# Kernel tuning notes

Hardware: AMD Instinct MI355X
Metric: run time of the kernel (lower is better)

The kernel has to match this reference:

```python
import jax, jax.numpy as jnp
import numpy as np

PERTURBATION_SCALE = 0.01

def setup_inputs() -> dict:
    key = jax.random.key(0)
    k1, k2, k3 = jax.random.split(key, 3)
    theta = jax.random.normal(k1, (256, 512), dtype=jnp.float32)
    basis_eval = jax.random.normal(k2, (100000, 512), dtype=jnp.float32)
    noise = jax.random.normal(k3, (256, 512), dtype=jnp.float32)
    return {"theta": theta, "basis_eval": basis_eval, "noise": noise}

def reference(theta, basis_eval, noise):
    # phi: [N, K] functional evaluations
    phi_raw = basis_eval @ theta.T
    phi_perturbed = basis_eval @ (theta + noise * PERTURBATION_SCALE).T
    # sign-crossings between consecutive evaluation points: [N-1, K]
    crossings = (phi_raw[:-1] * phi_raw[1:] < 0).astype(theta.dtype)
    crossings_p = (phi_perturbed[:-1] * phi_perturbed[1:] < 0).astype(theta.dtype)
    persistence = crossings * crossings_p  # [N-1, K]
    # fused pairwise shared-persistence: Gram matrix [K, K]
    gram = persistence.T @ persistence
    K = theta.shape[0]
    iu, ju = jnp.triu_indices(K, k=1)  # row-major i<j == itertools.combinations order
    return gram[iu, ju]  # [K*(K-1)/2]
```

## Files before the change

kernel.cpp:

```cpp
#include <hip/hip_runtime.h>
#include <hip/hip_bf16.h>
#include <stdint.h>

#define N_PTS   100000
#define D       512
#define KDIM    256
#define NB1     99999
#define NWORDS  1564
#define NW      1563
#define GRIDX   3128
#define CHUNK   391

typedef float  f32x4  __attribute__((ext_vector_type(4)));
typedef __bf16 bf16x8 __attribute__((ext_vector_type(8)));

__global__ void build_w(const float* __restrict__ theta,
                        const float* __restrict__ noise,
                        __bf16* __restrict__ W) {
    int idx = blockIdx.x * 256 + threadIdx.x;
    int j = idx >> 9;
    int d = idx & 511;
    float v;
    if (j < KDIM) v = theta[j * D + d];
    else          v = theta[(j - KDIM) * D + d] + 0.01f * noise[(j - KDIM) * D + d];
    W[idx] = (__bf16)v;
}

__global__ void __launch_bounds__(256)
gemm_signs(const float* __restrict__ basis,
           const __bf16* __restrict__ W,
           uint64_t* __restrict__ sbits) {
    __shared__ char smem[17024];
    __bf16* As = (__bf16*)smem;
    __bf16* Bs = (__bf16*)(smem + 8192);

    const int tid  = threadIdx.x;
    const int lane = tid & 63;
    const int wave = tid >> 6;
    const int wrow = wave >> 1;
    const int wcol = wave & 1;

    const int phys = blockIdx.x;
    const int lid  = (phys & 7) * CHUNK + (phys >> 3);
    const int bn   = lid & 3;
    const int bm   = lid >> 2;

    const int srow  = tid >> 1;
    const int shalf = tid & 1;
    int agrow = bm * 128 + srow;
    if (agrow > N_PTS - 1) agrow = N_PTS - 1;
    const float*  aptr = basis + (size_t)agrow * D + shalf * 16;
    const __bf16* bptr = W + (size_t)(bn * 128 + srow) * D + shalf * 16;

    f32x4 acc[4][4] = {};
    float4 ra[2][4];
    uint4  rb[2][2];

    {
        const float4* ap = (const float4*)aptr;
        ra[0][0] = ap[0]; ra[0][1] = ap[1]; ra[0][2] = ap[2]; ra[0][3] = ap[3];
        const uint4* bp = (const uint4*)bptr;
        rb[0][0] = bp[0]; rb[0][1] = bp[1];
    }

    const int lane16 = lane & 15;
    const int lgrp   = lane >> 4;
    const int aoff   = (wrow * 64 + lane16) * 32 + lgrp * 8;
    const int boff   = (wcol * 64 + lane16) * 32 + lgrp * 8;

    #pragma unroll
    for (int kt = 0; kt < 16; ++kt) {
        const int cur = kt & 1, nxt = cur ^ 1;

        if (kt < 15) {
            const float4* ap = (const float4*)(aptr + (size_t)(kt + 1) * 32);
            ra[nxt][0] = ap[0]; ra[nxt][1] = ap[1]; ra[nxt][2] = ap[2]; ra[nxt][3] = ap[3];
            const uint4* bp = (const uint4*)(bptr + (size_t)(kt + 1) * 32);
            rb[nxt][0] = bp[0]; rb[nxt][1] = bp[1];
        }

        __bf16 abuf[16];
        #pragma unroll
        for (int v = 0; v < 4; ++v) {
            abuf[v * 4 + 0] = (__bf16)ra[cur][v].x;
            abuf[v * 4 + 1] = (__bf16)ra[cur][v].y;
            abuf[v * 4 + 2] = (__bf16)ra[cur][v].z;
            abuf[v * 4 + 3] = (__bf16)ra[cur][v].w;
        }

        __builtin_amdgcn_s_barrier();
        {
            bf16x8* adst = (bf16x8*)&As[srow * 32 + shalf * 16];
            adst[0] = *(bf16x8*)&abuf[0];
            adst[1] = *(bf16x8*)&abuf[8];
            uint4* bdst = (uint4*)&Bs[srow * 32 + shalf * 16];
            bdst[0] = rb[cur][0];
            bdst[1] = rb[cur][1];
        }
        asm volatile("s_waitcnt lgkmcnt(0)" ::: "memory");
        __builtin_amdgcn_s_barrier();
        __builtin_amdgcn_sched_barrier(0);

        bf16x8 af[4], bfm[4];
        #pragma unroll
        for (int m = 0; m < 4; ++m) af[m]  = *(bf16x8*)&As[aoff + m * 512];
        #pragma unroll
        for (int n = 0; n < 4; ++n) bfm[n] = *(bf16x8*)&Bs[boff + n * 512];

        #pragma unroll
        for (int m = 0; m < 4; ++m)
            #pragma unroll
            for (int n = 0; n < 4; ++n)
                acc[m][n] = __builtin_amdgcn_mfma_f32_16x16x32_bf16(af[m], bfm[n], acc[m][n], 0, 0, 0);
    }

    __builtin_amdgcn_s_barrier();
    unsigned char* sb = (unsigned char*)smem;

    #pragma unroll
    for (int m = 0; m < 4; ++m) {
        #pragma unroll
        for (int n = 0; n < 4; ++n) {
            const int cl  = wcol * 64 + n * 16 + lane16;
            const int rw  = wrow * 64 + m * 16 + lgrp * 4;
            uint32_t pk = 0;
            #pragma unroll
            for (int r = 0; r < 4; ++r)
                pk |= (acc[m][n][r] < 0.0f ? 1u : 0u) << (8 * r);
            *(uint32_t*)&sb[cl * 132 + rw] = pk;
        }
    }
    asm volatile("s_waitcnt lgkmcnt(0)" ::: "memory");
    __builtin_amdgcn_s_barrier();

    {
        const int col  = tid >> 1;
        const int half = tid & 1;
        const unsigned char* src = &sb[col * 132 + half * 64];
        uint64_t wbits = 0;
        #pragma unroll
        for (int k = 0; k < 16; ++k) {
            uint32_t q  = *(const uint32_t*)&src[4 * k];
            uint32_t p4 = ((q & 0x01010101u) * 0x10204080u) >> 28;
            wbits |= (uint64_t)p4 << (4 * k);
        }
        sbits[(size_t)(bm * 2 + half) * 512 + bn * 128 + col] = wbits;
    }
}

__global__ void crossing_masks(const uint64_t* __restrict__ sbits,
                               uint64_t* __restrict__ maskT) {
    const int w = blockIdx.x;
    const int j = threadIdx.x;
    uint64_t s0r = sbits[(size_t)w * 512 + j];
    uint64_t s0p = sbits[(size_t)w * 512 + 256 + j];
    uint64_t s1r = sbits[(size_t)(w + 1) * 512 + j];
    uint64_t s1p = sbits[(size_t)(w + 1) * 512 + 256 + j];
    uint64_t cr = s0r ^ ((s0r >> 1) | (s1r << 63));
    uint64_t cp = s0p ^ ((s0p >> 1) | (s1p << 63));
    uint64_t m = cr & cp;
    if (w == NW - 1) m &= 0x7FFFFFFFull;
    maskT[(size_t)w * 256 + j] = m;
}

__global__ void zero_out(float* __restrict__ out) {
    int i = blockIdx.x * 256 + threadIdx.x;
    if (i < 32640) out[i] = 0.0f;
}

__global__ void pair_popcount(const uint64_t* __restrict__ maskT,
                              float* __restrict__ out) {
    const int i = blockIdx.x;
    const int c = blockIdx.y;
    const int j = threadIdx.x;
    if (j <= i) return;
    int w0 = c * 391;
    int w1 = w0 + 391; if (w1 > NW) w1 = NW;
    uint32_t sum = 0;
    #pragma unroll 4
    for (int w = w0; w < w1; ++w) {
        uint64_t mi = maskT[(size_t)w * 256 + i];
        uint64_t mj = maskT[(size_t)w * 256 + j];
        sum += (uint32_t)__popcll(mi & mj);
    }
    const size_t idx = (size_t)i * (2 * KDIM - i - 1) / 2 + (size_t)(j - i - 1);
    atomicAdd(&out[idx], (float)sum);
}

extern "C" void kernel_launch(void* const* d_in, const int* in_sizes, int n_in,
                              void* d_out, int out_size, void* d_ws, size_t ws_size,
                              hipStream_t stream) {
    const float* theta = (const float*)d_in[0];
    const float* basis = (const float*)d_in[1];
    const float* noise = (const float*)d_in[2];
    float* out = (float*)d_out;

    char* ws = (char*)d_ws;
    __bf16*   W     = (__bf16*)ws;
    uint64_t* sbits = (uint64_t*)(ws + 524288);
    uint64_t* maskT = (uint64_t*)(ws + 524288 + (size_t)NWORDS * 512 * 8);

    hipLaunchKernelGGL(build_w,        dim3(1024),    dim3(256), 0, stream, theta, noise, W);
    hipLaunchKernelGGL(gemm_signs,     dim3(GRIDX),   dim3(256), 0, stream, basis, W, sbits);
    hipLaunchKernelGGL(crossing_masks, dim3(NW),      dim3(256), 0, stream, sbits, maskT);
    hipLaunchKernelGGL(zero_out,       dim3(128),     dim3(256), 0, stream, out);
    hipLaunchKernelGGL(pair_popcount,  dim3(KDIM, 4), dim3(256), 0, stream, maskT, out);
}
```

Baseline: 143.2 us.

## Load GEMM fragments directly from global memory into registers, bypassing LDS staging

```diff
diff --git a/kernel.cpp b/kernel.cpp
--- a/kernel.cpp
+++ b/kernel.cpp
@@ -5,7 +5,6 @@
 #define N_PTS   100000
 #define D       512
 #define KDIM    256
-#define NB1     99999
 #define NWORDS  1564
 #define NW      1563
 #define GRIDX   3128
@@ -26,13 +25,11 @@
     W[idx] = (__bf16)v;
 }
 
-__global__ void __launch_bounds__(256)
+__global__ void __launch_bounds__(256, 2)
 gemm_signs(const float* __restrict__ basis,
            const __bf16* __restrict__ W,
            uint64_t* __restrict__ sbits) {
-    __shared__ char smem[17024];
-    __bf16* As = (__bf16*)smem;
-    __bf16* Bs = (__bf16*)(smem + 8192);
+    __shared__ unsigned char sb[128 * 132];
 
     const int tid  = threadIdx.x;
     const int lane = tid & 63;
@@ -45,67 +42,64 @@
     const int bn   = lid & 3;
     const int bm   = lid >> 2;
 
-    const int srow  = tid >> 1;
-    const int shalf = tid & 1;
-    int agrow = bm * 128 + srow;
-    if (agrow > N_PTS - 1) agrow = N_PTS - 1;
-    const float*  aptr = basis + (size_t)agrow * D + shalf * 16;
-    const __bf16* bptr = W + (size_t)(bn * 128 + srow) * D + shalf * 16;
+    const int lane16 = lane & 15;
+    const int lgrp   = lane >> 4;
 
-    f32x4 acc[4][4] = {};
-    float4 ra[2][4];
-    uint4  rb[2][2];
-
-    {
-        const float4* ap = (const float4*)aptr;
-        ra[0][0] = ap[0]; ra[0][1] = ap[1]; ra[0][2] = ap[2]; ra[0][3] = ap[3];
-        const uint4* bp = (const uint4*)bptr;
-        rb[0][0] = bp[0]; rb[0][1] = bp[1];
+    const float*  ap[4];
+    const __bf16* bp[4];
+    #pragma unroll
+    for (int m = 0; m < 4; ++m) {
+        int r = bm * 128 + wrow * 64 + m * 16 + lane16;
+        if (r > N_PTS - 1) r = N_PTS - 1;
+        ap[m] = basis + (size_t)r * D + lgrp * 8;
+    }
+    #pragma unroll
+    for (int n = 0; n < 4; ++n) {
+        int c = bn * 128 + wcol * 64 + n * 16 + lane16;
+        bp[n] = W + (size_t)c * D + lgrp * 8;
     }
 
-    const int lane16 = lane & 15;
-    const int lgrp   = lane >> 4;
-    const int aoff   = (wrow * 64 + lane16) * 32 + lgrp * 8;
-    const int boff   = (wcol * 64 + lane16) * 32 + lgrp * 8;
+    f32x4  acc[4][4] = {};
+    float4 ra[2][4][2];
+    uint4  rb[2][4];
+
+    #pragma unroll
+    for (int m = 0; m < 4; ++m) {
+        ra[0][m][0] = *(const float4*)(ap[m]);
+        ra[0][m][1] = *(const float4*)(ap[m] + 4);
+    }
+    #pragma unroll
+    for (int n = 0; n < 4; ++n) rb[0][n] = *(const uint4*)(bp[n]);
 
     #pragma unroll
     for (int kt = 0; kt < 16; ++kt) {
         const int cur = kt & 1, nxt = cur ^ 1;
 
         if (kt < 15) {
-            const float4* ap = (const float4*)(aptr + (size_t)(kt + 1) * 32);
-            ra[nxt][0] = ap[0]; ra[nxt][1] = ap[1]; ra[nxt][2] = ap[2]; ra[nxt][3] = ap[3];
-            const uint4* bp = (const uint4*)(bptr + (size_t)(kt + 1) * 32);
-            rb[nxt][0] = bp[0]; rb[nxt][1] = bp[1];
+            #pragma unroll
+            for (int m = 0; m < 4; ++m) {
+                ra[nxt][m][0] = *(const float4*)(ap[m] + (kt + 1) * 32);
+                ra[nxt][m][1] = *(const float4*)(ap[m] + (kt + 1) * 32 + 4);
+            }
+            #pragma unroll
+            for (int n = 0; n < 4; ++n)
+                rb[nxt][n] = *(const uint4*)(bp[n] + (kt + 1) * 32);
         }
-
-        __bf16 abuf[16];
-        #pragma unroll
-        for (int v = 0; v < 4; ++v) {
-            abuf[v * 4 + 0] = (__bf16)ra[cur][v].x;
-            abuf[v * 4 + 1] = (__bf16)ra[cur][v].y;
-            abuf[v * 4 + 2] = (__bf16)ra[cur][v].z;
-            abuf[v * 4 + 3] = (__bf16)ra[cur][v].w;
-        }
-
-        __builtin_amdgcn_s_barrier();
-        {
-            bf16x8* adst = (bf16x8*)&As[srow * 32 + shalf * 16];
-            adst[0] = *(bf16x8*)&abuf[0];
-            adst[1] = *(bf16x8*)&abuf[8];
-            uint4* bdst = (uint4*)&Bs[srow * 32 + shalf * 16];
-            bdst[0] = rb[cur][0];
-            bdst[1] = rb[cur][1];
-        }
-        asm volatile("s_waitcnt lgkmcnt(0)" ::: "memory");
-        __builtin_amdgcn_s_barrier();
-        __builtin_amdgcn_sched_barrier(0);
 
         bf16x8 af[4], bfm[4];
         #pragma unroll
-        for (int m = 0; m < 4; ++m) af[m]  = *(bf16x8*)&As[aoff + m * 512];
+        for (int m = 0; m < 4; ++m) {
+            af[m][0] = (__bf16)ra[cur][m][0].x;
+            af[m][1] = (__bf16)ra[cur][m][0].y;
+            af[m][2] = (__bf16)ra[cur][m][0].z;
+            af[m][3] = (__bf16)ra[cur][m][0].w;
+            af[m][4] = (__bf16)ra[cur][m][1].x;
+            af[m][5] = (__bf16)ra[cur][m][1].y;
+            af[m][6] = (__bf16)ra[cur][m][1].z;
+            af[m][7] = (__bf16)ra[cur][m][1].w;
+        }
         #pragma unroll
-        for (int n = 0; n < 4; ++n) bfm[n] = *(bf16x8*)&Bs[boff + n * 512];
+        for (int n = 0; n < 4; ++n) bfm[n] = *(bf16x8*)&rb[cur][n];
 
         #pragma unroll
         for (int m = 0; m < 4; ++m)
@@ -114,15 +108,12 @@
                 acc[m][n] = __builtin_amdgcn_mfma_f32_16x16x32_bf16(af[m], bfm[n], acc[m][n], 0, 0, 0);
     }
 
-    __builtin_amdgcn_s_barrier();
-    unsigned char* sb = (unsigned char*)smem;
-
     #pragma unroll
     for (int m = 0; m < 4; ++m) {
         #pragma unroll
         for (int n = 0; n < 4; ++n) {
-            const int cl  = wcol * 64 + n * 16 + lane16;
-            const int rw  = wrow * 64 + m * 16 + lgrp * 4;
+            const int cl = wcol * 64 + n * 16 + lane16;
+            const int rw = wrow * 64 + m * 16 + lgrp * 4;
             uint32_t pk = 0;
             #pragma unroll
             for (int r = 0; r < 4; ++r)
@@ -130,8 +121,7 @@
             *(uint32_t*)&sb[cl * 132 + rw] = pk;
         }
     }
-    asm volatile("s_waitcnt lgkmcnt(0)" ::: "memory");
-    __builtin_amdgcn_s_barrier();
+    __syncthreads();
 
     {
         const int col  = tid >> 1;
```

Result: slower. 340.8 us (+138.0%).
